# Performance work log

Measured on AMD Instinct MI355X. Metric: run time of the kernel, lower is better.

The kernel has to match this reference:

```python
import jax, jax.numpy as jnp
import numpy as np

DIM = 64
HEADS = 4
WIN = 4


def setup_inputs() -> dict:
    key = jax.random.key(0)
    ks = jax.random.split(key, 9)
    B, C, D, H, W = 2, DIM, 64, 64, 64
    x = jax.random.normal(ks[0], (B, C, D, H, W), dtype=jnp.float32)
    # 1x1x1 Conv3d == pointwise linear: weight [C_out, C_in], bias [C_out]
    def mk(kw, kb):
        return (jax.random.normal(kw, (C, C), dtype=jnp.float32) * 0.05,
                jax.random.normal(kb, (C,), dtype=jnp.float32) * 0.05)
    Wq, bq = mk(ks[1], ks[2])
    Wk, bk = mk(ks[3], ks[4])
    Wv, bv = mk(ks[5], ks[6])
    Wp, bp = mk(ks[7], ks[8])
    return {"x": x, "Wq": Wq, "bq": bq, "Wk": Wk, "bk": bk,
            "Wv": Wv, "bv": bv, "Wp": Wp, "bp": bp}


def reference(x, Wq, bq, Wk, bk, Wv, bv, Wp, bp):
    B, C, D, H, W = x.shape
    w = WIN
    heads = HEADS
    hd = C // heads
    L = w * w * w  # tokens per window (64)
    nd, nh, nw = D // w, H // w, W // w  # spatial dims are multiples of w -> no padding branch
    scale = hd ** -0.5

    # window partition: [B,C,D,H,W] -> [B*nd*nh*nw, C, L]
    xw = (x.reshape(B, C, nd, w, nh, w, nw, w)
            .transpose(0, 2, 4, 6, 1, 3, 5, 7)
            .reshape(B * nd * nh * nw, C, L))

    def pointwise(t, Wm, bm):  # 1x1x1 conv on flattened windows
        return jnp.einsum('ncl,oc->nol', t, Wm) + bm[None, :, None]

    q = pointwise(xw, Wq, bq).reshape(-1, heads, hd, L)
    k = pointwise(xw, Wk, bk).reshape(-1, heads, hd, L)
    v = pointwise(xw, Wv, bv).reshape(-1, heads, hd, L)

    # attn[n,h,i,j] = <q[:, :, :, i], k[:, :, :, j]> * scale ; softmax over j
    attn = jax.nn.softmax(jnp.einsum('nhdi,nhdj->nhij', q, k) * scale, axis=-1)
    # out = v @ attn^T  (dropout is identity in eval)
    out = jnp.einsum('nhdj,nhij->nhdi', v, attn)

    out = out.reshape(-1, C, L)
    out = pointwise(out, Wp, bp)

    # reverse window partition: [B*nd*nh*nw, C, L] -> [B,C,D,H,W]
    out = (out.reshape(B, nd, nh, nw, C, w, w, w)
              .transpose(0, 4, 1, 5, 2, 6, 3, 7)
              .reshape(B, C, D, H, W))
    return out
```

## Files before the change

### kernel.cpp

```cpp
#include <hip/hip_runtime.h>

typedef _Float16 f16;
typedef __attribute__((ext_vector_type(4))) _Float16 f16x4;
typedef __attribute__((ext_vector_type(8))) _Float16 f16x8;
typedef __attribute__((ext_vector_type(4))) float f32x4;

#define MFMA32(a,b,c) __builtin_amdgcn_mfma_f32_16x16x32_f16((a),(b),(c),0,0,0)
#define MFMA16(a,b,c) __builtin_amdgcn_mfma_f32_16x16x16f16((a),(b),(c),0,0,0)

__global__ void wprep(const float* __restrict__ Wq, const float* __restrict__ Wk,
                      const float* __restrict__ Wv, const float* __restrict__ Wp,
                      f16* __restrict__ ws)
{
    const int t = threadIdx.x;
    const int lane = t & 63;
    const float* Wm[4] = {Wq, Wk, Wv, Wp};
    #pragma unroll
    for (int j = 0; j < 8; ++j) {
        const int c = (t >> 6) * 8 + j;
        const int m = c >> 3, ob = (c >> 1) & 3, s = c & 1;
        const float* src = Wm[m] + (ob * 16 + (lane & 15)) * 64 + 8 * (lane >> 4) + 32 * s;
        f32x4 a4 = *(const f32x4*)src;
        f32x4 b4 = *(const f32x4*)(src + 4);
        f16x8 h;
        #pragma unroll
        for (int ii = 0; ii < 8; ++ii) h[ii] = (f16)(ii < 4 ? a4[ii] : b4[ii - 4]);
        *(f16x8*)(ws + c * 512 + lane * 8) = h;
    }
}

__global__ __launch_bounds__(256, 3)
void wsa3d(const float* __restrict__ x, const f16* __restrict__ wsf,
           const float* __restrict__ bq, const float* __restrict__ bk,
           const float* __restrict__ bv, const float* __restrict__ bp,
           float* __restrict__ out)
{
    __shared__ __align__(16) f16 lds[16384];
    f16*   const XW = lds;
    float* const SG = (float*)lds;

    const int tid  = threadIdx.x;
    const int lane = tid & 63;
    const int w    = tid >> 6;
    const int g    = lane >> 4;
    const int ln16 = lane & 15;
    const int key  = ln16 & 7;

    const int bid = blockIdx.x;
    const int Q   = ((bid & 7) << 8) | (bid >> 3);
    const int qx = Q & 3, ih = (Q >> 2) & 15, idz = (Q >> 6) & 15, b = Q >> 10;

    const float c_sc = 0.25f * 1.44269504088896340736f;
    const f32x4 z4 = {0.f, 0.f, 0.f, 0.f};

    const int gz = (lane >> 4) & 3, gy = (lane >> 2) & 3, gq = lane & 3;

    f16x4 valh[16];
    #pragma unroll
    for (int i = 0; i < 16; ++i) {
        const int c = w * 16 + i;
        f32x4 v4 = *(const f32x4*)(x + ((((b*64 + c)*64 + idz*4 + gz)*64) + ih*4 + gy)*64 + qx*16 + gq*4);
        #pragma unroll
        for (int r = 0; r < 4; ++r) valh[i][r] = (f16)v4[r];
    }

    #pragma unroll
    for (int lx = 0; lx < 4; ++lx) {
        const int t = gz * 16 + gy * 4 + lx;
        #pragma unroll
        for (int h2 = 0; h2 < 2; ++h2) {
            f16x8 pk;
            #pragma unroll
            for (int ii = 0; ii < 8; ++ii) pk[ii] = valh[h2 * 8 + ii][lx];
            *(f16x8*)(XW + gq*4096 + t*64 + (((w*2 + h2) ^ (t & 7) ^ gq) << 3)) = pk;
        }
    }
    __syncthreads();

    f16x8 xf[4][2];
    #pragma unroll
    for (int lb = 0; lb < 4; ++lb)
        #pragma unroll
        for (int s = 0; s < 2; ++s)
            xf[lb][s] = *(const f16x8*)(XW + w*4096 + (lb*16 + ln16)*64 + (((g + 4*s) ^ key ^ w) << 3));

    #pragma unroll
    for (int ob = 0; ob < 4; ++ob) {
        f16x8 VF[2];
        #pragma unroll
        for (int s = 0; s < 2; ++s) VF[s] = *(const f16x8*)(wsf + (16 + ob*2 + s)*512 + lane*8);
        const float bvo = bv[ob * 16 + ln16];
        #pragma unroll
        for (int tb = 0; tb < 4; ++tb) {
            f32x4 a = z4;
            #pragma unroll
            for (int s = 0; s < 2; ++s) a = MFMA32(xf[tb][s], VF[s], a);
            f16x4 h4;
            #pragma unroll
            for (int r = 0; r < 4; ++r) h4[r] = (f16)(a[r] + bvo);
            *(f16x4*)(XW + w*4096 + (ob*16 + ln16)*64 + (((2*tb + (g >> 1)) ^ key ^ w) << 3) + 4*(g & 1)) = h4;
        }
    }

    f16x4 ot[4][4];
    #pragma unroll
    for (int h = 0; h < 4; ++h) {
        f16x8 QF[2], KF[2];
        #pragma unroll
        for (int s = 0; s < 2; ++s) {
            QF[s] = *(const f16x8*)(wsf + (h*2 + s)*512 + lane*8);
            KF[s] = *(const f16x8*)(wsf + (8 + h*2 + s)*512 + lane*8);
        }
        const f32x4 bqv = *(const f32x4*)(bq + h*16 + g*4);
        const f32x4 bkv = *(const f32x4*)(bk + h*16 + g*4);
        f16x4 qf[4], kf[4];
        #pragma unroll
        for (int lb = 0; lb < 4; ++lb) {
            f32x4 aq = z4, ak = z4;
            #pragma unroll
            for (int s = 0; s < 2; ++s) {
                aq = MFMA32(QF[s], xf[lb][s], aq);
                ak = MFMA32(KF[s], xf[lb][s], ak);
            }
            #pragma unroll
            for (int r = 0; r < 4; ++r) {
                qf[lb][r] = (f16)((aq[r] + bqv[r]) * c_sc);
                kf[lb][r] = (f16)(ak[r] + bkv[r]);
            }
        }
        f16x4 va[4];
        #pragma unroll
        for (int jb = 0; jb < 4; ++jb)
            va[jb] = *(const f16x4*)(XW + w*4096 + (16*h + ln16)*64 + (((2*jb + (g >> 1)) ^ key ^ w) << 3) + 4*(g & 1));
        #pragma unroll
        for (int ib = 0; ib < 4; ++ib) {
            f32x4 e[4];
            #pragma unroll
            for (int jb = 0; jb < 4; ++jb) {
                f32x4 S = MFMA16(kf[jb], qf[ib], z4);
                #pragma unroll
                for (int r = 0; r < 4; ++r) e[jb][r] = __builtin_amdgcn_exp2f(S[r]);
            }
            f32x4 s4 = e[0] + e[1] + e[2] + e[3];
            float hh = (s4[0] + s4[1]) + (s4[2] + s4[3]);
            hh += __shfl_xor(hh, 16);
            hh += __shfl_xor(hh, 32);
            const float inv = __builtin_amdgcn_rcpf(hh);
            f32x4 O = z4;
            #pragma unroll
            for (int jb = 0; jb < 4; ++jb) {
                f16x4 pf;
                #pragma unroll
                for (int r = 0; r < 4; ++r) pf[r] = (f16)e[jb][r];
                O = MFMA16(va[jb], pf, O);
            }
            #pragma unroll
            for (int r = 0; r < 4; ++r) ot[h][ib][r] = (f16)(O[r] * inv);
        }
    }

    #pragma unroll
    for (int h = 0; h < 4; ++h)
        #pragma unroll
        for (int ib = 0; ib < 4; ++ib)
            *(f16x4*)(XW + w*4096 + (16*ib + ln16)*64 + (((2*h + (g >> 1)) ^ key ^ w) << 3) + 4*(g & 1)) = ot[h][ib];

    f16x8 PF[4][2];
    #pragma unroll
    for (int oc = 0; oc < 4; ++oc)
        #pragma unroll
        for (int s = 0; s < 2; ++s) PF[oc][s] = *(const f16x8*)(wsf + (24 + oc*2 + s)*512 + lane*8);
    float bps[4];
    #pragma unroll
    for (int oc = 0; oc < 4; ++oc) bps[oc] = bp[oc * 16 + ln16];

    f32x4 res[4][4];
    #pragma unroll
    for (int tb = 0; tb < 4; ++tb) {
        f16x8 af[2];
        #pragma unroll
        for (int s = 0; s < 2; ++s)
            af[s] = *(const f16x8*)(XW + w*4096 + (tb*16 + ln16)*64 + (((g + 4*s) ^ key ^ w) << 3));
        #pragma unroll
        for (int oc = 0; oc < 4; ++oc) {
            f32x4 a = z4;
            #pragma unroll
            for (int s = 0; s < 2; ++s) a = MFMA32(af[s], PF[oc][s], a);
            #pragma unroll
            for (int r = 0; r < 4; ++r) res[tb][oc][r] = a[r] + bps[oc];
        }
    }
    __syncthreads();

    #pragma unroll
    for (int oc = 0; oc < 4; ++oc) {
        #pragma unroll
        for (int tb = 0; tb < 4; ++tb)
            *(f32x4*)(SG + w*1092 + ln16*68 + ((tb*16 + g*4) ^ (w << 2))) = res[tb][oc];
        __syncthreads();
        #pragma unroll
        for (int si = 0; si < 4; ++si) {
            const int o2 = w * 4 + si;
            f32x4 v4 = *(const f32x4*)(SG + gq*1092 + o2*68 + ((gz*16 + gy*4) ^ (gq << 2)));
            *(f32x4*)(out + ((((b*64 + oc*16 + o2)*64 + idz*4 + gz)*64) + ih*4 + gy)*64 + qx*16 + gq*4) = v4;
        }
        if (oc < 3) __syncthreads();
    }
}

extern "C" void kernel_launch(void* const* d_in, const int* in_sizes, int n_in,
                              void* d_out, int out_size, void* d_ws, size_t ws_size,
                              hipStream_t stream) {
    (void)in_sizes; (void)n_in; (void)out_size; (void)ws_size;
    const float* x  = (const float*)d_in[0];
    const float* Wq = (const float*)d_in[1];
    const float* bq = (const float*)d_in[2];
    const float* Wk = (const float*)d_in[3];
    const float* bk = (const float*)d_in[4];
    const float* Wv = (const float*)d_in[5];
    const float* bv = (const float*)d_in[6];
    const float* Wp = (const float*)d_in[7];
    const float* bp = (const float*)d_in[8];
    f16* wsf = (f16*)d_ws;
    wprep<<<1, 256, 0, stream>>>(Wq, Wk, Wv, Wp, wsf);
    wsa3d<<<2048, 256, 0, stream>>>(x, wsf, bq, bk, bv, bp, (float*)d_out);
}
```

Measured before the change: 67.64 us.

## Stream attention output straight to LDS and transpose projection to cut registers

Each head's attention output is now written straight to shared memory as it is produced, instead of being held in a 4x4 register array until all heads finish. The final projection is transposed so the weights are the A operand and the activations, read element-wise from a channel-major swizzled LDS layout, are the B operand. This also changes the staging stores to scalar writes. Launch bounds are raised to 4 blocks per CU to exploit the lower register pressure. The trade-off is many scalar 2-byte LDS reads and writes, with possible bank conflicts, in place of vector accesses.

```diff
diff --git a/kernel.cpp b/kernel.cpp
--- a/kernel.cpp
+++ b/kernel.cpp
@@ -29,7 +29,7 @@
     }
 }
 
-__global__ __launch_bounds__(256, 3)
+__global__ __launch_bounds__(256, 4)
 void wsa3d(const float* __restrict__ x, const f16* __restrict__ wsf,
            const float* __restrict__ bq, const float* __restrict__ bk,
            const float* __restrict__ bv, const float* __restrict__ bp,
@@ -102,7 +102,6 @@
         }
     }
 
-    f16x4 ot[4][4];
     #pragma unroll
     for (int h = 0; h < 4; ++h) {
         f16x8 QF[2], KF[2];
@@ -134,60 +133,60 @@
             va[jb] = *(const f16x4*)(XW + w*4096 + (16*h + ln16)*64 + (((2*jb + (g >> 1)) ^ key ^ w) << 3) + 4*(g & 1));
         #pragma unroll
         for (int ib = 0; ib < 4; ++ib) {
-            f32x4 e[4];
+            f16x4 pf[4];
+            f32x4 s4 = z4;
             #pragma unroll
             for (int jb = 0; jb < 4; ++jb) {
                 f32x4 S = MFMA16(kf[jb], qf[ib], z4);
                 #pragma unroll
-                for (int r = 0; r < 4; ++r) e[jb][r] = __builtin_amdgcn_exp2f(S[r]);
-            }
-            f32x4 s4 = e[0] + e[1] + e[2] + e[3];
+                for (int r = 0; r < 4; ++r) {
+                    float ev = __builtin_amdgcn_exp2f(S[r]);
+                    pf[jb][r] = (f16)ev;
+                    s4[r] += ev;
+                }
+            }
             float hh = (s4[0] + s4[1]) + (s4[2] + s4[3]);
             hh += __shfl_xor(hh, 16);
             hh += __shfl_xor(hh, 32);
             const float inv = __builtin_amdgcn_rcpf(hh);
             f32x4 O = z4;
             #pragma unroll
-            for (int jb = 0; jb < 4; ++jb) {
-                f16x4 pf;
-                #pragma unroll
-                for (int r = 0; r < 4; ++r) pf[r] = (f16)e[jb][r];
-                O = MFMA16(va[jb], pf, O);
-            }
-            #pragma unroll
-            for (int r = 0; r < 4; ++r) ot[h][ib][r] = (f16)(O[r] * inv);
-        }
-    }
-
-    #pragma unroll
-    for (int h = 0; h < 4; ++h)
-        #pragma unroll
-        for (int ib = 0; ib < 4; ++ib)
-            *(f16x4*)(XW + w*4096 + (16*ib + ln16)*64 + (((2*h + (g >> 1)) ^ key ^ w) << 3) + 4*(g & 1)) = ot[h][ib];
-
-    f16x8 PF[4][2];
+            for (int jb = 0; jb < 4; ++jb) O = MFMA16(va[jb], pf[jb], O);
+            #pragma unroll
+            for (int r = 0; r < 4; ++r) {
+                const int row = 16*h + 4*g + r;
+                XW[w*4096 + row*64 + ((16*ib + ln16) ^ ((4*g + r) << 1))] = (f16)(O[r] * inv);
+            }
+        }
+    }
+
+    f16x8 PFr[4][2];
     #pragma unroll
     for (int oc = 0; oc < 4; ++oc)
         #pragma unroll
-        for (int s = 0; s < 2; ++s) PF[oc][s] = *(const f16x8*)(wsf + (24 + oc*2 + s)*512 + lane*8);
-    float bps[4];
-    #pragma unroll
-    for (int oc = 0; oc < 4; ++oc) bps[oc] = bp[oc * 16 + ln16];
+        for (int s = 0; s < 2; ++s) PFr[oc][s] = *(const f16x8*)(wsf + (24 + oc*2 + s)*512 + lane*8);
+    f32x4 bpv[4];
+    #pragma unroll
+    for (int oc = 0; oc < 4; ++oc) bpv[oc] = *(const f32x4*)(bp + oc*16 + 4*g);
 
     f32x4 res[4][4];
     #pragma unroll
     for (int tb = 0; tb < 4; ++tb) {
-        f16x8 af[2];
+        f16x8 bf[2];
         #pragma unroll
         for (int s = 0; s < 2; ++s)
-            af[s] = *(const f16x8*)(XW + w*4096 + (tb*16 + ln16)*64 + (((g + 4*s) ^ key ^ w) << 3));
+            #pragma unroll
+            for (int ii = 0; ii < 8; ++ii) {
+                const int c = 8*g + 32*s + ii;
+                bf[s][ii] = XW[w*4096 + c*64 + ((16*tb + ln16) ^ (((8*g + ii) & 15) << 1))];
+            }
         #pragma unroll
         for (int oc = 0; oc < 4; ++oc) {
             f32x4 a = z4;
-            #pragma unroll
-            for (int s = 0; s < 2; ++s) a = MFMA32(af[s], PF[oc][s], a);
-            #pragma unroll
-            for (int r = 0; r < 4; ++r) res[tb][oc][r] = a[r] + bps[oc];
+            a = MFMA32(PFr[oc][0], bf[0], a);
+            a = MFMA32(PFr[oc][1], bf[1], a);
+            #pragma unroll
+            for (int r = 0; r < 4; ++r) res[tb][oc][r] = a[r] + bpv[oc][r];
         }
     }
     __syncthreads();
@@ -196,7 +195,9 @@
     for (int oc = 0; oc < 4; ++oc) {
         #pragma unroll
         for (int tb = 0; tb < 4; ++tb)
-            *(f32x4*)(SG + w*1092 + ln16*68 + ((tb*16 + g*4) ^ (w << 2))) = res[tb][oc];
+            #pragma unroll
+            for (int r = 0; r < 4; ++r)
+                SG[w*1092 + (4*g + r)*68 + ((16*tb + ln16) ^ (w << 2))] = res[tb][oc][r];
         __syncthreads();
         #pragma unroll
         for (int si = 0; si < 4; ++si) {
```

Measured after the change: 72.59 us. 7.3% more time.
